# Performance work log

Measured on AMD Instinct MI355X. Metric: run time of the kernel, lower is better.

Reference implementation:

```python
import jax, jax.numpy as jnp
import numpy as np

ANCHORS = np.array([[116., 90.], [156., 198.], [373., 326.],
                    [30., 61.], [62., 45.], [59., 119.],
                    [10., 13.], [16., 30.], [33., 23.]], dtype=np.float32)
IMG_WH = (416.0, 416.0)  # image_size[::-1]
IGNORE_THRESH = 0.5
MAX_BOXES = 64  # static upper bound on true boxes per image per layer


def bce_logits(t, x):
    # tf.nn.sigmoid_cross_entropy_with_logits(labels=t, logits=x)
    return jnp.maximum(x, 0.0) - x * t + jnp.log1p(jnp.exp(-jnp.abs(x)))


def box_iou(b1, b2):
    # b1: [B,H,W,3,4] xywh, b2: [B,M,4] xywh -> iou [B,H,W,3,M]
    b1 = b1[..., None, :]
    b2 = b2[:, None, None, None, :, :]
    b1_min = b1[..., :2] - b1[..., 2:4] * 0.5
    b1_max = b1[..., :2] + b1[..., 2:4] * 0.5
    b2_min = b2[..., :2] - b2[..., 2:4] * 0.5
    b2_max = b2[..., :2] + b2[..., 2:4] * 0.5
    inter_wh = jnp.maximum(jnp.minimum(b1_max, b2_max) - jnp.maximum(b1_min, b2_min), 0.0)
    inter = inter_wh[..., 0] * inter_wh[..., 1]
    a1 = b1[..., 2] * b1[..., 3]
    a2 = b2[..., 2] * b2[..., 3]
    return inter / (a1 + a2 - inter)


def layer_loss(yt, pred, anchors):
    # yt: [B,H,W,3,5+C], pred: [B,H,W,3*(5+C)]
    B, H, W = yt.shape[:3]
    C = pred.shape[-1] // 3 - 5
    p = pred.reshape(B, H, W, 3, 5 + C)
    gy, gx = jnp.meshgrid(jnp.arange(H), jnp.arange(W), indexing='ij')
    grid = jnp.stack([gx, gy], -1).astype(pred.dtype)[:, :, None, :]  # [H,W,1,2]
    fwh = jnp.array([W, H], pred.dtype)
    anc = anchors.reshape(1, 1, 1, 3, 2)
    # pred_process (channel layout: 0=conf, 1:3=xy, 3:5=wh, 5:=class)
    xy = (jax.nn.sigmoid(p[..., 1:3]) + grid) / fwh
    wh = jnp.exp(p[..., 3:5]) * anc / fwh
    conf = jax.nn.sigmoid(p[..., 0:1])
    cls = jax.nn.sigmoid(p[..., 5:])
    pred_box = jnp.concatenate([xy, wh], -1)

    obj = yt[..., 0:1]
    true_cls = yt[..., 5:]
    true_xy = yt[..., 1:3] * fwh - grid
    true_wh = jnp.log(yt[..., 3:5] / anc * jnp.array(IMG_WH, yt.dtype))
    true_wh = jnp.where(obj > 0, true_wh, jnp.zeros_like(true_wh))
    scale = 2.0 - yt[..., 3:4] * yt[..., 4:5]

    # vectorized replacement for the per-image while_loop + boolean_mask:
    # gather the MAX_BOXES highest-objectness cells per image as candidate true boxes
    flat_obj = obj[..., 0].reshape(B, -1)
    flat_box = yt[..., 1:5].reshape(B, -1, 4)
    vals, idx = jax.lax.top_k(flat_obj, MAX_BOXES)
    tboxes = jnp.take_along_axis(flat_box, idx[..., None], axis=1)  # [B,M,4]
    iou = box_iou(pred_box, tboxes)                                 # [B,H,W,3,M]
    iou = jnp.where((vals > 0.5)[:, None, None, None, :], iou, -jnp.inf)
    best_iou = jnp.max(iou, axis=-1)  # -inf when no true boxes (matches tf reduce_max over empty)
    ignore = (best_iou < IGNORE_THRESH).astype(yt.dtype)[..., None]

    xy_l = obj * scale * bce_logits(true_xy, xy)
    wh_l = obj * scale * 0.5 * jnp.square(true_wh - wh)
    conf_l = obj * bce_logits(obj, conf) + (1.0 - obj) * bce_logits(obj, conf) * ignore
    cls_l = obj * bce_logits(true_cls, cls)
    red = lambda t: jnp.sum(t, axis=(1, 2, 3, 4))
    return red(xy_l) + red(wh_l) + red(conf_l) + red(cls_l)


def yolo_loss(y_true, p0, p1, p2):
    B, _, A, D = y_true.shape
    yts = [y_true[:, 0:169].reshape(B, 13, 13, A, D),
           y_true[:, 169:845].reshape(B, 26, 26, A, D),
           y_true[:, 845:3549].reshape(B, 52, 52, A, D)]
    anc = jnp.asarray(ANCHORS)
    total = jnp.zeros((B,), y_true.dtype)
    for i, pred in enumerate([p0, p1, p2]):
        total = total + layer_loss(yts[i], pred, anc[3 * i:3 * i + 3])
    return total


def setup_inputs() -> dict:
    key = jax.random.key(0)
    B, N, C = 32, 3549, 80
    k1, k2, k3, k4, k5, k6, k7 = jax.random.split(key, 7)
    obj = (jax.random.uniform(k1, (B, N, 3, 1)) < 0.002).astype(jnp.float32)
    xy = jax.random.uniform(k2, (B, N, 3, 2), minval=0.05, maxval=0.95)
    wh = jax.random.uniform(k3, (B, N, 3, 2), minval=0.05, maxval=0.4)
    cls = (jax.random.uniform(k4, (B, N, 3, C)) < (1.0 / C)).astype(jnp.float32)
    y_true = jnp.concatenate([obj, xy, wh, cls], axis=-1)
    pred_13 = 0.5 * jax.random.normal(k5, (B, 13, 13, 255), dtype=jnp.float32)
    pred_26 = 0.5 * jax.random.normal(k6, (B, 26, 26, 255), dtype=jnp.float32)
    pred_52 = 0.5 * jax.random.normal(k7, (B, 52, 52, 255), dtype=jnp.float32)
    return {"y_true": y_true, "pred_13": pred_13, "pred_26": pred_26, "pred_52": pred_52}


def reference(y_true, pred_13, pred_26, pred_52):
    return yolo_loss(y_true, pred_13, pred_26, pred_52)
```

## Files before the change

### kernel.cpp

```cpp
#include <hip/hip_runtime.h>

#define MAXB 64
#define CAP 256
#define BLK_PER_BATCH 6

__constant__ float c_anc[9][2] = {
    {116.f, 90.f}, {156.f, 198.f}, {373.f, 326.f},
    { 30.f, 61.f}, { 62.f, 45.f}, { 59.f, 119.f},
    { 10.f, 13.f}, { 16.f, 30.f}, { 33.f, 23.f}};

typedef float floatx4 __attribute__((ext_vector_type(4), aligned(4)));

__device__ __forceinline__ float sigm(float x) {
    return __builtin_amdgcn_rcpf(1.f + __expf(-x));
}
__device__ __forceinline__ float bce_f(float t, float x) {
    return fmaxf(x, 0.f) - x * t + __logf(1.f + __expf(-fabsf(x)));
}

__global__ void init_k(float* __restrict__ out) { out[threadIdx.x] = 0.f; }

template <int ITERS>
__device__ __forceinline__ void scan_obj(const float* __restrict__ ybase,
                                         int nCells, int nwords, int lane,
                                         int wv, unsigned long long* swords) {
    float ov[ITERS];
#pragma unroll
    for (int k = 0; k < ITERS; ++k) {
        int wi = k * 16 + wv;
        int c = (wi << 6) + lane;
        ov[k] = (wi < nwords && c < nCells) ? ybase[(long long)c * 85] : 0.f;
    }
#pragma unroll
    for (int k = 0; k < ITERS; ++k) {
        int wi = k * 16 + wv;
        unsigned long long m = __ballot(ov[k] > 0.5f);
        if (lane == 0 && wi < nwords) swords[wi] = m;
    }
}

__global__ __launch_bounds__(1024) void loss_k(
    const float* __restrict__ yt,
    const float* __restrict__ p13, const float* __restrict__ p26,
    const float* __restrict__ p52, float* __restrict__ out)
{
    int bid = blockIdx.x, tid = threadIdx.x;
    int b = bid / BLK_PER_BATCH, j = bid - b * BLK_PER_BATCH;
    int l, blk, S, n0, nwords, start, cnt;
    if (j == 0)      { l = 0; blk = 0;     S = 13; n0 = 0;   nwords = 8;   start = 0;              cnt = 507;  }
    else if (j == 1) { l = 1; blk = 0;     S = 26; n0 = 169; nwords = 32;  start = 0;              cnt = 2028; }
    else             { l = 2; blk = j - 2; S = 52; n0 = 845; nwords = 128; start = (j - 2) * 2028; cnt = 2028; }
    int nCells = S * S * 3;
    float Sf = (float)S;
    float invS = __builtin_amdgcn_rcpf(Sf);
    const float* ybase = yt + (long long)(b * 3549 + n0) * 255;
    const float* pred  = (l == 0) ? p13 : (l == 1) ? p26 : p52;
    const float* pbase = pred + (long long)b * S * S * 255;
    int lane = tid & 63, wv = tid >> 6;

    int c0 = start + tid;
    int c1 = start + tid + 1024;
    bool act0 = (tid < cnt) && (c0 < nCells);
    bool act1 = (tid + 1024 < cnt) && (c1 < nCells);
    int cc0 = act0 ? c0 : 0, cc1 = act1 ? c1 : 0;
    const float* pp0 = pbase + (long long)cc0 * 85;
    const float* pp1 = pbase + (long long)cc1 * 85;
    floatx4 v03_0 = *(const floatx4*)pp0;
    float v4_0 = pp0[4];
    floatx4 v03_1 = *(const floatx4*)pp1;
    float v4_1 = pp1[4];

    __shared__ unsigned long long swords[128];
    __shared__ int sidx[CAP];
    __shared__ int sbase2[2];
    __shared__ int stot_s;
    __shared__ float sxmin[MAXB], sxmax[MAXB], symin[MAXB], symax[MAXB], sba[MAXB];

    if (l == 0)      scan_obj<1>(ybase, nCells, nwords, lane, wv, swords);
    else if (l == 1) scan_obj<2>(ybase, nCells, nwords, lane, wv, swords);
    else             scan_obj<8>(ybase, nCells, nwords, lane, wv, swords);
    __syncthreads();

    unsigned long long w = 0ULL;
    int pc = 0;
    if (tid < 128) { w = (tid < nwords) ? swords[tid] : 0ULL; pc = __popcll(w); }
    int x = pc;
#pragma unroll
    for (int d = 1; d < 64; d <<= 1) {
        int y = __shfl_up(x, d, 64);
        if (lane >= d) x += y;
    }
    if (tid < 128 && lane == 63) sbase2[wv] = x;
    __syncthreads();
    if (tid == 0) stot_s = sbase2[0] + sbase2[1];
    if (tid < 128) {
        int base = x - pc + (wv ? sbase2[0] : 0);
        unsigned long long ww = w;
        while (ww) {
            int bit = __ffsll((long long)ww) - 1;
            if (base < CAP) sidx[base] = tid * 64 + bit;
            ++base;
            ww &= ww - 1;
        }
    }
    __syncthreads();

    int stot = stot_s;
    int TC = stot < CAP ? stot : CAP;
    int MB = TC < MAXB ? TC : MAXB;
    if (tid < MB) {
        int idx = sidx[tid];
        if (idx >= nCells) idx = nCells - 1;
        const float* yc = ybase + (long long)idx * 85;
        float gx = yc[1], gy = yc[2], gww = yc[3], ghh = yc[4];
        sxmin[tid] = gx - gww * 0.5f; sxmax[tid] = gx + gww * 0.5f;
        symin[tid] = gy - ghh * 0.5f; symax[tid] = gy + ghh * 0.5f;
        sba[tid]   = gww * ghh;
    }
    __syncthreads();

    float loss = 0.f;
#pragma unroll
    for (int it = 0; it < 2; ++it) {
        int cc = it ? cc1 : cc0;
        bool act = it ? act1 : act0;
        floatx4 v03 = it ? v03_1 : v03_0;
        float v4 = it ? v4_1 : v4_0;

        int p_ = cc / 3, a = cc - p_ * 3;
        int gh = p_ / S, gw = p_ - gh * S;
        float aw = c_anc[l * 3 + a][0], ah = c_anc[l * 3 + a][1];
        float px = (sigm(v03.y) + (float)gw) * invS;
        float py = (sigm(v03.z) + (float)gh) * invS;
        float pw = __expf(v03.w) * aw * invS, ph = __expf(v4) * ah * invS;
        float pxmin = px - pw * 0.5f, pxmax = px + pw * 0.5f;
        float pymin = py - ph * 0.5f, pymax = py + ph * 0.5f;
        float parea = pw * ph;
        bool hit = false;
        for (int i = 0; i < MB; ++i) {
            float iw = fminf(pxmax, sxmax[i]) - fmaxf(pxmin, sxmin[i]);
            float ih = fminf(pymax, symax[i]) - fmaxf(pymin, symin[i]);
            float inter = fmaxf(iw, 0.f) * fmaxf(ih, 0.f);
            hit = hit || (3.f * inter >= parea + sba[i]);
        }
        bool posbit = (swords[cc >> 6] >> (cc & 63)) & 1ULL;
        float conf = sigm(v03.x);
        float bval = fmaxf(conf, 0.f) + __logf(1.f + __expf(-fabsf(conf)));
        loss += (act && !posbit && !hit) ? bval : 0.f;
    }

    if (blk == 0) {
        float wsum = 0.f;
        for (int i = wv; i < TC; i += 16) {
            int idx = sidx[i];
            if (idx >= nCells) idx = nCells - 1;
            const float* yc = ybase + (long long)idx * 85;
            const float* pp = pbase + (long long)idx * 85;
            float part = bce_f(yc[5 + lane], sigm(pp[5 + lane]));
            if (lane < 16)
                part += bce_f(yc[69 + lane], sigm(pp[69 + lane]));
            if (lane == 0) {
                int q = idx / 3, aa = idx - q * 3;
                int qh = q / S, qw = q - qh * S;
                float aw2 = c_anc[l * 3 + aa][0], ah2 = c_anc[l * 3 + aa][1];
                float t1 = yc[1], t2 = yc[2], t3 = yc[3], t4 = yc[4];
                float u0 = pp[0], u1 = pp[1], u2 = pp[2], u3 = pp[3], u4 = pp[4];
                part += bce_f(1.f, sigm(u0));
                float sc = 2.f - t3 * t4;
                float qx = (sigm(u1) + (float)qw) * invS;
                float qy = (sigm(u2) + (float)qh) * invS;
                part += sc * (bce_f(t1 * Sf - (float)qw, qx) +
                              bce_f(t2 * Sf - (float)qh, qy));
                float qpw = __expf(u3) * aw2 * invS;
                float qph = __expf(u4) * ah2 * invS;
                float twx = __logf(t3 / aw2 * 416.f);
                float twy = __logf(t4 / ah2 * 416.f);
                part += sc * 0.5f *
                        ((twx - qpw) * (twx - qpw) + (twy - qph) * (twy - qph));
            }
#pragma unroll
            for (int off = 32; off > 0; off >>= 1)
                part += __shfl_down(part, off, 64);
            if (lane == 0) wsum += part;
        }
        if (lane == 0) loss += wsum;
    }

#pragma unroll
    for (int off = 32; off > 0; off >>= 1)
        loss += __shfl_down(loss, off, 64);
    __shared__ float wred[16];
    if (lane == 0) wred[wv] = loss;
    __syncthreads();
    if (tid == 0) {
        float s = 0.f;
#pragma unroll
        for (int k = 0; k < 16; ++k) s += wred[k];
        atomicAdd(out + b, s);
    }
}

extern "C" void kernel_launch(void* const* d_in, const int* in_sizes, int n_in,
                              void* d_out, int out_size, void* d_ws, size_t ws_size,
                              hipStream_t stream) {
    (void)in_sizes; (void)n_in; (void)out_size; (void)d_ws; (void)ws_size;
    const float* yt  = (const float*)d_in[0];
    const float* p13 = (const float*)d_in[1];
    const float* p26 = (const float*)d_in[2];
    const float* p52 = (const float*)d_in[3];
    float* out = (float*)d_out;

    init_k<<<1, 32, 0, stream>>>(out);
    loss_k<<<32 * BLK_PER_BATCH, 1024, 0, stream>>>(yt, p13, p26, p52, out);
}
```

Before: 236.1 us.

## Cut blocks per batch to four and template per-layer bodies with more cells per thread

Work per image drops from six blocks to four: the 52x52 layer is now split into two halves with four cells per thread instead of four quarters with two. Each layer path is templated so sizes and loop counts are compile-time constants, and the true-box read becomes a single vector load. This means the 52x52 objectness scan and box gather are repeated across fewer blocks, at the cost of fewer blocks in flight (128 on a large GPU) and more serial work per thread.

```diff
diff --git a/kernel.cpp b/kernel.cpp
--- a/kernel.cpp
+++ b/kernel.cpp
@@ -2,7 +2,6 @@
 
 #define MAXB 64
 #define CAP 256
-#define BLK_PER_BATCH 6
 
 __constant__ float c_anc[9][2] = {
     {116.f, 90.f}, {156.f, 198.f}, {373.f, 326.f},
@@ -20,139 +19,127 @@
 
 __global__ void init_k(float* __restrict__ out) { out[threadIdx.x] = 0.f; }
 
-template <int ITERS>
-__device__ __forceinline__ void scan_obj(const float* __restrict__ ybase,
-                                         int nCells, int nwords, int lane,
-                                         int wv, unsigned long long* swords) {
-    float ov[ITERS];
-#pragma unroll
-    for (int k = 0; k < ITERS; ++k) {
+struct SmemT {
+    unsigned long long swords[128];
+    int sidx[CAP];
+    int sbase2[2];
+    int stot_s;
+    float sxmin[MAXB], sxmax[MAXB], symin[MAXB], symax[MAXB], sba[MAXB];
+    float wred[16];
+};
+
+template <int SC, int PR, int L>
+__device__ __forceinline__ void pair_body(
+    int b, int half, const float* __restrict__ yt,
+    const float* __restrict__ pred, float* __restrict__ out,
+    SmemT& sm, int tid, int lane, int wv)
+{
+    constexpr int S      = (L == 0) ? 13 : (L == 1) ? 26  : 52;
+    constexpr int n0     = (L == 0) ? 0  : (L == 1) ? 169 : 845;
+    constexpr int nwords = (L == 0) ? 8  : (L == 1) ? 32  : 128;
+    constexpr int nCells = S * S * 3;
+    constexpr int halfSz = (L == 2) ? 4056 : nCells;
+    const float Sf = (float)S;
+    const float invS = 1.f / Sf;
+    const float* ybase = yt + (long long)(b * 3549 + n0) * 255;
+    const float* pbase = pred + (long long)b * S * S * 255;
+
+    float ov[SC];
+#pragma unroll
+    for (int k = 0; k < SC; ++k) {
         int wi = k * 16 + wv;
         int c = (wi << 6) + lane;
         ov[k] = (wi < nwords && c < nCells) ? ybase[(long long)c * 85] : 0.f;
     }
-#pragma unroll
-    for (int k = 0; k < ITERS; ++k) {
+
+    int start = half * halfSz;
+    bool act[PR]; int cc[PR]; floatx4 v03[PR]; float v4[PR];
+#pragma unroll
+    for (int i = 0; i < PR; ++i) {
+        int c = start + tid + i * 1024;
+        bool a = (tid + i * 1024 < halfSz) && (c < nCells);
+        act[i] = a; cc[i] = a ? c : 0;
+        const float* pp = pbase + (long long)cc[i] * 85;
+        v03[i] = *(const floatx4*)pp;
+        v4[i]  = pp[4];
+    }
+
+#pragma unroll
+    for (int k = 0; k < SC; ++k) {
         int wi = k * 16 + wv;
         unsigned long long m = __ballot(ov[k] > 0.5f);
-        if (lane == 0 && wi < nwords) swords[wi] = m;
-    }
-}
-
-__global__ __launch_bounds__(1024) void loss_k(
-    const float* __restrict__ yt,
-    const float* __restrict__ p13, const float* __restrict__ p26,
-    const float* __restrict__ p52, float* __restrict__ out)
-{
-    int bid = blockIdx.x, tid = threadIdx.x;
-    int b = bid / BLK_PER_BATCH, j = bid - b * BLK_PER_BATCH;
-    int l, blk, S, n0, nwords, start, cnt;
-    if (j == 0)      { l = 0; blk = 0;     S = 13; n0 = 0;   nwords = 8;   start = 0;              cnt = 507;  }
-    else if (j == 1) { l = 1; blk = 0;     S = 26; n0 = 169; nwords = 32;  start = 0;              cnt = 2028; }
-    else             { l = 2; blk = j - 2; S = 52; n0 = 845; nwords = 128; start = (j - 2) * 2028; cnt = 2028; }
-    int nCells = S * S * 3;
-    float Sf = (float)S;
-    float invS = __builtin_amdgcn_rcpf(Sf);
-    const float* ybase = yt + (long long)(b * 3549 + n0) * 255;
-    const float* pred  = (l == 0) ? p13 : (l == 1) ? p26 : p52;
-    const float* pbase = pred + (long long)b * S * S * 255;
-    int lane = tid & 63, wv = tid >> 6;
-
-    int c0 = start + tid;
-    int c1 = start + tid + 1024;
-    bool act0 = (tid < cnt) && (c0 < nCells);
-    bool act1 = (tid + 1024 < cnt) && (c1 < nCells);
-    int cc0 = act0 ? c0 : 0, cc1 = act1 ? c1 : 0;
-    const float* pp0 = pbase + (long long)cc0 * 85;
-    const float* pp1 = pbase + (long long)cc1 * 85;
-    floatx4 v03_0 = *(const floatx4*)pp0;
-    float v4_0 = pp0[4];
-    floatx4 v03_1 = *(const floatx4*)pp1;
-    float v4_1 = pp1[4];
-
-    __shared__ unsigned long long swords[128];
-    __shared__ int sidx[CAP];
-    __shared__ int sbase2[2];
-    __shared__ int stot_s;
-    __shared__ float sxmin[MAXB], sxmax[MAXB], symin[MAXB], symax[MAXB], sba[MAXB];
-
-    if (l == 0)      scan_obj<1>(ybase, nCells, nwords, lane, wv, swords);
-    else if (l == 1) scan_obj<2>(ybase, nCells, nwords, lane, wv, swords);
-    else             scan_obj<8>(ybase, nCells, nwords, lane, wv, swords);
+        if (lane == 0 && wi < nwords) sm.swords[wi] = m;
+    }
     __syncthreads();
 
     unsigned long long w = 0ULL;
     int pc = 0;
-    if (tid < 128) { w = (tid < nwords) ? swords[tid] : 0ULL; pc = __popcll(w); }
+    if (tid < 128) { w = (tid < nwords) ? sm.swords[tid] : 0ULL; pc = __popcll(w); }
     int x = pc;
 #pragma unroll
     for (int d = 1; d < 64; d <<= 1) {
         int y = __shfl_up(x, d, 64);
         if (lane >= d) x += y;
     }
-    if (tid < 128 && lane == 63) sbase2[wv] = x;
-    __syncthreads();
-    if (tid == 0) stot_s = sbase2[0] + sbase2[1];
+    if (tid < 128 && lane == 63) sm.sbase2[wv] = x;
+    __syncthreads();
+    if (tid == 0) sm.stot_s = sm.sbase2[0] + sm.sbase2[1];
     if (tid < 128) {
-        int base = x - pc + (wv ? sbase2[0] : 0);
+        int base = x - pc + (wv ? sm.sbase2[0] : 0);
         unsigned long long ww = w;
         while (ww) {
             int bit = __ffsll((long long)ww) - 1;
-            if (base < CAP) sidx[base] = tid * 64 + bit;
+            if (base < CAP) sm.sidx[base] = tid * 64 + bit;
             ++base;
             ww &= ww - 1;
         }
     }
     __syncthreads();
 
-    int stot = stot_s;
+    int stot = sm.stot_s;
     int TC = stot < CAP ? stot : CAP;
     int MB = TC < MAXB ? TC : MAXB;
     if (tid < MB) {
-        int idx = sidx[tid];
+        int idx = sm.sidx[tid];
         if (idx >= nCells) idx = nCells - 1;
         const float* yc = ybase + (long long)idx * 85;
-        float gx = yc[1], gy = yc[2], gww = yc[3], ghh = yc[4];
-        sxmin[tid] = gx - gww * 0.5f; sxmax[tid] = gx + gww * 0.5f;
-        symin[tid] = gy - ghh * 0.5f; symax[tid] = gy + ghh * 0.5f;
-        sba[tid]   = gww * ghh;
+        floatx4 g = *(const floatx4*)(yc + 1);
+        sm.sxmin[tid] = g.x - g.z * 0.5f; sm.sxmax[tid] = g.x + g.z * 0.5f;
+        sm.symin[tid] = g.y - g.w * 0.5f; sm.symax[tid] = g.y + g.w * 0.5f;
+        sm.sba[tid]   = g.z * g.w;
     }
     __syncthreads();
 
     float loss = 0.f;
 #pragma unroll
-    for (int it = 0; it < 2; ++it) {
-        int cc = it ? cc1 : cc0;
-        bool act = it ? act1 : act0;
-        floatx4 v03 = it ? v03_1 : v03_0;
-        float v4 = it ? v4_1 : v4_0;
-
-        int p_ = cc / 3, a = cc - p_ * 3;
+    for (int i = 0; i < PR; ++i) {
+        int c = cc[i];
+        int p_ = c / 3, a = c - p_ * 3;
         int gh = p_ / S, gw = p_ - gh * S;
-        float aw = c_anc[l * 3 + a][0], ah = c_anc[l * 3 + a][1];
-        float px = (sigm(v03.y) + (float)gw) * invS;
-        float py = (sigm(v03.z) + (float)gh) * invS;
-        float pw = __expf(v03.w) * aw * invS, ph = __expf(v4) * ah * invS;
+        float aw = c_anc[L * 3 + a][0], ah = c_anc[L * 3 + a][1];
+        float px = (sigm(v03[i].y) + (float)gw) * invS;
+        float py = (sigm(v03[i].z) + (float)gh) * invS;
+        float pw = __expf(v03[i].w) * aw * invS, ph = __expf(v4[i]) * ah * invS;
         float pxmin = px - pw * 0.5f, pxmax = px + pw * 0.5f;
         float pymin = py - ph * 0.5f, pymax = py + ph * 0.5f;
         float parea = pw * ph;
         bool hit = false;
-        for (int i = 0; i < MB; ++i) {
-            float iw = fminf(pxmax, sxmax[i]) - fmaxf(pxmin, sxmin[i]);
-            float ih = fminf(pymax, symax[i]) - fmaxf(pymin, symin[i]);
+        for (int k = 0; k < MB; ++k) {
+            float iw = fminf(pxmax, sm.sxmax[k]) - fmaxf(pxmin, sm.sxmin[k]);
+            float ih = fminf(pymax, sm.symax[k]) - fmaxf(pymin, sm.symin[k]);
             float inter = fmaxf(iw, 0.f) * fmaxf(ih, 0.f);
-            hit = hit || (3.f * inter >= parea + sba[i]);
+            hit = hit || (3.f * inter >= parea + sm.sba[k]);
         }
-        bool posbit = (swords[cc >> 6] >> (cc & 63)) & 1ULL;
-        float conf = sigm(v03.x);
+        bool posbit = (sm.swords[c >> 6] >> (c & 63)) & 1ULL;
+        float conf = sigm(v03[i].x);
         float bval = fmaxf(conf, 0.f) + __logf(1.f + __expf(-fabsf(conf)));
-        loss += (act && !posbit && !hit) ? bval : 0.f;
-    }
-
-    if (blk == 0) {
+        loss += (act[i] && !posbit && !hit) ? bval : 0.f;
+    }
+
+    if (half == 0) {
         float wsum = 0.f;
         for (int i = wv; i < TC; i += 16) {
-            int idx = sidx[i];
+            int idx = sm.sidx[i];
             if (idx >= nCells) idx = nCells - 1;
             const float* yc = ybase + (long long)idx * 85;
             const float* pp = pbase + (long long)idx * 85;
@@ -162,7 +149,7 @@
             if (lane == 0) {
                 int q = idx / 3, aa = idx - q * 3;
                 int qh = q / S, qw = q - qh * S;
-                float aw2 = c_anc[l * 3 + aa][0], ah2 = c_anc[l * 3 + aa][1];
+                float aw2 = c_anc[L * 3 + aa][0], ah2 = c_anc[L * 3 + aa][1];
                 float t1 = yc[1], t2 = yc[2], t3 = yc[3], t4 = yc[4];
                 float u0 = pp[0], u1 = pp[1], u2 = pp[2], u3 = pp[3], u4 = pp[4];
                 part += bce_f(1.f, sigm(u0));
@@ -189,15 +176,31 @@
 #pragma unroll
     for (int off = 32; off > 0; off >>= 1)
         loss += __shfl_down(loss, off, 64);
-    __shared__ float wred[16];
-    if (lane == 0) wred[wv] = loss;
+    if (lane == 0) sm.wred[wv] = loss;
     __syncthreads();
     if (tid == 0) {
         float s = 0.f;
 #pragma unroll
-        for (int k = 0; k < 16; ++k) s += wred[k];
+        for (int k = 0; k < 16; ++k) s += sm.wred[k];
         atomicAdd(out + b, s);
     }
+}
+
+__global__ __launch_bounds__(1024) void loss_k(
+    const float* __restrict__ yt,
+    const float* __restrict__ p13, const float* __restrict__ p26,
+    const float* __restrict__ p52, float* __restrict__ out)
+{
+    __shared__ SmemT sm;
+    int bid = blockIdx.x, tid = threadIdx.x;
+    int b = bid >> 2, j = bid & 3;
+    int lane = tid & 63, wv = tid >> 6;
+    if (j == 0)
+        pair_body<1, 1, 0>(b, 0, yt, p13, out, sm, tid, lane, wv);
+    else if (j == 1)
+        pair_body<2, 2, 1>(b, 0, yt, p26, out, sm, tid, lane, wv);
+    else
+        pair_body<8, 4, 2>(b, j - 2, yt, p52, out, sm, tid, lane, wv);
 }
 
 extern "C" void kernel_launch(void* const* d_in, const int* in_sizes, int n_in,
@@ -211,5 +214,5 @@
     float* out = (float*)d_out;
 
     init_k<<<1, 32, 0, stream>>>(out);
-    loss_k<<<32 * BLK_PER_BATCH, 1024, 0, stream>>>(yt, p13, p26, p52, out);
-}
+    loss_k<<<32 * 4, 1024, 0, stream>>>(yt, p13, p26, p52, out);
+}
```

Measured after the change: 243.1 us. +3.0%, slower.
